# Kernel optimization log

Measured on AMD Instinct MI355X. Metric: run time of the kernel, lower is better.

## Reference

```python
import jax, jax.numpy as jnp
import numpy as np

DIM = 16
HID = 256
BATCH = 8192
N_STEPS = 10      # fixed-step RK4 replaces adaptive dopri5 for a deterministic reference
T0, T1 = 0.0, 1.0
LOG_2PI = float(np.log(2.0 * np.pi))


def setup_inputs() -> dict:
    key = jax.random.key(0)
    ks = jax.random.split(key, 7)

    def lin_w(k, fan_in, fan_out):
        lim = 1.0 / np.sqrt(fan_in)
        return jax.random.uniform(k, (fan_in, fan_out), minval=-lim, maxval=lim, dtype=jnp.float32)

    def lin_b(k, fan_in, fan_out):
        lim = 1.0 / np.sqrt(fan_in)
        return jax.random.uniform(k, (fan_out,), minval=-lim, maxval=lim, dtype=jnp.float32)

    x = jax.random.normal(ks[0], (BATCH, DIM), dtype=jnp.float32)
    return {
        "x": x,
        "W1": lin_w(ks[1], DIM + 1, HID), "b1": lin_b(ks[2], DIM + 1, HID),
        "W2": lin_w(ks[3], HID, HID),     "b2": lin_b(ks[4], HID, HID),
        "W3": lin_w(ks[5], HID, DIM),     "b3": lin_b(ks[6], HID, DIM),
    }


def _mlp(W1, b1, W2, b2, W3, b3, h):
    h = jax.nn.silu(h @ W1 + b1)
    h = jax.nn.silu(h @ W2 + b2)
    return h @ W3 + b3


def reference(x, W1, b1, W2, b2, W3, b3):
    dtype = x.dtype

    def f(t, z):  # time-conditioned vector field f(z, t): [B, d] -> [B, d]
        t_col = jnp.full((z.shape[0], 1), t, dtype=dtype)
        return _mlp(W1, b1, W2, b2, W3, b3, jnp.concatenate([z, t_col], axis=1))

    eye = jnp.eye(DIM, dtype=dtype)

    def f_and_div(t, z):
        fz = f(t, z)
        # exact divergence = trace of Jacobian, via DIM forward-mode JVPs
        def jvp_dir(e):  # e: [d]
            _, jv = jax.jvp(lambda zz: f(t, zz), (z,), (jnp.broadcast_to(e, z.shape),))
            return jv  # [B, d]
        jvs = jax.vmap(jvp_dir)(eye)          # [d, B, d]
        div = jnp.einsum('ibi->b', jvs)       # sum_i dF_i/dz_i
        return fz, div

    dt = jnp.asarray((T1 - T0) / N_STEPS, dtype=dtype)

    def rhs(t, z):
        fz, div = f_and_div(t, z)
        return fz, -div   # dz/dt, dlogp/dt

    def step(state, i):
        z, logp = state
        t = T0 + i * dt
        k1z, k1l = rhs(t, z)
        k2z, k2l = rhs(t + 0.5 * dt, z + 0.5 * dt * k1z)
        k3z, k3l = rhs(t + 0.5 * dt, z + 0.5 * dt * k2z)
        k4z, k4l = rhs(t + dt, z + dt * k3z)
        z = z + (dt / 6.0) * (k1z + 2.0 * k2z + 2.0 * k3z + k4z)
        logp = logp + (dt / 6.0) * (k1l + 2.0 * k2l + 2.0 * k3l + k4l)
        return (z, logp), None

    logp0 = jnp.zeros(x.shape[0], dtype=dtype)
    (z1, logp1), _ = jax.lax.scan(step, (x, logp0), jnp.arange(N_STEPS, dtype=dtype))

    logpz = -0.5 * (jnp.sum(z1 * z1, axis=1) + DIM * LOG_2PI)
    return logpz - logp1
```

## Files before the change

kernel.cpp:

```cpp
#include <hip/hip_runtime.h>

#define DIM 16
#define HID 256
#define NSTEPS 10
#define TILE_B 32
#define NTHR 1024
#define LSH 264

typedef __attribute__((ext_vector_type(8))) short bf16x8;
typedef __attribute__((ext_vector_type(4))) float f32x4;
typedef __attribute__((ext_vector_type(2))) unsigned int u32x2;

__device__ __forceinline__ unsigned short f2bf(float f) {
    unsigned u = __float_as_uint(f);
    u += 0x7fff + ((u >> 16) & 1);
    return (unsigned short)(u >> 16);
}
__device__ __forceinline__ float bfw_lo(unsigned u) { return __uint_as_float(u << 16); }
__device__ __forceinline__ float bfw_hi(unsigned u) { return __uint_as_float(u & 0xffff0000u); }
__device__ __forceinline__ unsigned packtr(float a, float b) {
    return __builtin_amdgcn_perm(__float_as_uint(b), __float_as_uint(a), 0x07060302u);
}
__device__ __forceinline__ void silu_both(float x, float& h, float& d) {
    float s = __builtin_amdgcn_rcpf(1.0f + __expf(-x));
    h = x * s;
    d = fmaf(h, 1.0f - s, s);
}

__global__ void cnf_setup(const float* __restrict__ W1, const float* __restrict__ W2,
                          const float* __restrict__ W3,
                          unsigned short* __restrict__ w2t, unsigned short* __restrict__ mt) {
    const int j = blockIdx.x;
    const int n = threadIdx.x;
    float g = 0.0f;
#pragma unroll
    for (int i = 0; i < DIM; ++i) g = fmaf(W1[i * HID + j], W3[n * DIM + i], g);
    const float w2 = W2[j * HID + n];
    w2t[n * HID + j] = f2bf(w2);
    mt [n * HID + j] = f2bf(w2 * g);
}

__global__ __launch_bounds__(NTHR, 4) void cnf_main(
    const float* __restrict__ x,
    const float* __restrict__ W1, const float* __restrict__ b1,
    const float* __restrict__ b2, const float* __restrict__ b3,
    const unsigned short* __restrict__ w2t, const unsigned short* __restrict__ mt,
    const float* __restrict__ W3, float* __restrict__ out)
{
    __shared__ unsigned short zb[TILE_B][40];
    __shared__ unsigned short w3t[DIM][LSH];
    __shared__ unsigned short h1s[TILE_B][LSH];
    __shared__ unsigned short d1s[TILE_B][LSH];
    __shared__ unsigned short h2s[TILE_B][LSH];
    __shared__ unsigned short d2s[TILE_B][LSH];
    __shared__ float divp[8][TILE_B];
    __shared__ float b2l[HID];
    __shared__ float b3l[DIM];

    const int tid  = (int)threadIdx.x;
    const int lane = tid & 63;
    const int wv   = tid >> 6;
    const int g    = lane >> 4;
    const int r    = lane & 15;
    const int g8   = g * 8;
    const int b0   = (int)blockIdx.x * TILE_B;
    const int swr  = ((r >> 3) & 1) << 4;
    const int zsw  = ((r >> 3) & 1) << 3;
    const int goff = g8 ^ swr;
    const int n0w  = (wv & 7) * 32;

    bf16x8 breg[8][2];
    {
        const unsigned short* Bg = (wv < 8) ? w2t : mt;
#pragma unroll
        for (int k = 0; k < 8; ++k)
#pragma unroll
            for (int nt = 0; nt < 2; ++nt)
                breg[k][nt] = *(const bf16x8*)(Bg + (n0w + nt * 16 + r) * HID + k * 32 + g8);
    }

    bf16x8 w1f;
    {
        const int n = wv * 16 + r;
#pragma unroll
        for (int e = 0; e < 8; ++e) {
            const int k = g8 + e;
            float v = 0.0f;
            if (k < 17)       v = W1[k * HID + n];
            else if (k == 17) v = b1[n];
            w1f[e] = (short)f2bf(v);
        }
    }

    float zb4[4] = {0, 0, 0, 0}, za4[4] = {0, 0, 0, 0};
    if (wv < 2) {
        const f32x4 xv = *(const f32x4*)&x[(b0 + wv * 16 + r) * DIM + 4 * g];
#pragma unroll
        for (int q = 0; q < 4; ++q) zb4[q] = xv[q];
        u32x2 pz = { (unsigned)f2bf(zb4[0]) | ((unsigned)f2bf(zb4[1]) << 16),
                     (unsigned)f2bf(zb4[2]) | ((unsigned)f2bf(zb4[3]) << 16) };
        *(u32x2*)&zb[wv * 16 + r][(4 * g) ^ zsw] = pz;
    }
    if (tid < TILE_B) {
        const int zswi = ((tid >> 3) & 1) << 3;
#pragma unroll
        for (int c = 16; c < 32; ++c)
            zb[tid][c ^ zswi] = (c == 17) ? (unsigned short)0x3F80 : (unsigned short)0;
    }
    if (tid < 512) {
        const int n = tid >> 5, k0 = (tid & 31) * 8;
#pragma unroll
        for (int j = 0; j < 8; ++j) w3t[n][k0 + j] = f2bf(W3[(k0 + j) * DIM + n]);
    }
    if (tid < HID) b2l[tid] = b2[tid];
    if (tid < DIM) b3l[tid] = b3[tid];

    float lacc = 0.0f, logp = 0.0f;
    const float dt = 0.1f, dt6 = dt / 6.0f;

    for (int it = 0; it < NSTEPS * 4; ++it) {
        const int s = it & 3;
        const float wst = (s == 1 || s == 2) ? 2.0f : 1.0f;
        int opq = 0;
        asm volatile("" : "+v"(opq));
        __syncthreads();

        if (wv == 8 && lane < TILE_B && it) {
            const int ps = (it + 3) & 3;
            const float pw = (ps == 1 || ps == 2) ? 2.0f : 1.0f;
            float dv = 0.0f;
#pragma unroll
            for (int w = 0; w < 8; ++w) dv += divp[w][lane];
            lacc = fmaf(-pw, dv, lacc);
            if (ps == 3) { logp = fmaf(dt6, lacc, logp); lacc = 0.0f; }
        }

        {
            const bf16x8 bz0 = *(const bf16x8*)&zb[r][g8 ^ zsw];
            const bf16x8 bz1 = *(const bf16x8*)&zb[16 + r][g8 ^ zsw];
#pragma unroll
            for (int bt = 0; bt < 2; ++bt) {
                f32x4 c = {0.f, 0.f, 0.f, 0.f};
                c = __builtin_amdgcn_mfma_f32_16x16x32_bf16(w1f, bt ? bz1 : bz0, c, 0, 0, 0);
                float h[4], d[4];
#pragma unroll
                for (int q = 0; q < 4; ++q) silu_both(c[q], h[q], d[q]);
                const int row = bt * 16 + r;
                const int col = (wv * 16 + 4 * g) ^ swr;
                u32x2 hv  = { packtr(h[0], h[1]), packtr(h[2], h[3]) };
                u32x2 dv2 = { packtr(d[0], d[1]), packtr(d[2], d[3]) };
                *(u32x2*)&h1s[row][col] = hv;
                *(u32x2*)&d1s[row][col] = dv2;
            }
        }
        __syncthreads();

        f32x4 cc[2][2];
        {
            const unsigned short (*aT)[LSH] = (wv < 8) ? h1s : d1s;
#pragma unroll
            for (int a = 0; a < 2; ++a)
#pragma unroll
                for (int b = 0; b < 2; ++b) cc[a][b] = (f32x4){0.f, 0.f, 0.f, 0.f};
            __builtin_amdgcn_s_setprio(1);
#pragma unroll
            for (int k = 0; k < 8; ++k) {
                bf16x8 af[2];
#pragma unroll
                for (int bt = 0; bt < 2; ++bt)
                    af[bt] = *(const bf16x8*)&aT[bt * 16 + r][k * 32 + goff];
#pragma unroll
                for (int nt = 0; nt < 2; ++nt)
#pragma unroll
                    for (int bt = 0; bt < 2; ++bt)
                        cc[nt][bt] = __builtin_amdgcn_mfma_f32_16x16x32_bf16(breg[k][nt], af[bt], cc[nt][bt], 0, 0, 0);
            }
            __builtin_amdgcn_s_setprio(0);
        }
        if (wv < 8) {
#pragma unroll
            for (int nt = 0; nt < 2; ++nt) {
                const f32x4* bp2 = (const f32x4*)&b2l[n0w + nt * 16 + 4 * g];
                const f32x4 bb = bp2[opq];
#pragma unroll
                for (int bt = 0; bt < 2; ++bt) {
                    float h[4], d[4];
#pragma unroll
                    for (int q = 0; q < 4; ++q) silu_both(cc[nt][bt][q] + bb[q], h[q], d[q]);
                    const int row = bt * 16 + r;
                    const int col = (n0w + nt * 16 + 4 * g) ^ swr;
                    u32x2 hv  = { packtr(h[0], h[1]), packtr(h[2], h[3]) };
                    u32x2 dv2 = { packtr(d[0], d[1]), packtr(d[2], d[3]) };
                    *(u32x2*)&h2s[row][col] = hv;
                    *(u32x2*)&d2s[row][col] = dv2;
                }
            }
        }
        __syncthreads();

        if (wv < 2) {
            __builtin_amdgcn_s_setprio(1);
            const unsigned short* h2row = &h2s[wv * 16 + r][0];
            const unsigned short* w3row = &w3t[r][0];
            f32x4 c3a = {0.f, 0.f, 0.f, 0.f}, c3b = {0.f, 0.f, 0.f, 0.f};
#pragma unroll
            for (int kt = 0; kt < 8; ++kt) {
                const bf16x8 a3  = *(const bf16x8*)(w3row + kt * 32 + g8);
                const bf16x8 bf3 = *(const bf16x8*)(h2row + kt * 32 + goff);
                if (kt & 1) c3b = __builtin_amdgcn_mfma_f32_16x16x32_bf16(a3, bf3, c3b, 0, 0, 0);
                else        c3a = __builtin_amdgcn_mfma_f32_16x16x32_bf16(a3, bf3, c3a, 0, 0, 0);
            }
            const f32x4* bp3 = (const f32x4*)&b3l[4 * g];
            const f32x4 b3v = bp3[opq];
            const float coef = (s == 2) ? dt : 0.5f * dt;
            float zn[4];
#pragma unroll
            for (int q = 0; q < 4; ++q) {
                const float fz = c3a[q] + c3b[q] + b3v[q];
                za4[q] = fmaf(wst, fz, za4[q]);
                if (s < 3) zn[q] = fmaf(coef, fz, zb4[q]);
                else { zb4[q] = fmaf(dt6, za4[q], zb4[q]); zn[q] = zb4[q]; za4[q] = 0.0f; }
            }
            u32x2 pz = { (unsigned)f2bf(zn[0]) | ((unsigned)f2bf(zn[1]) << 16),
                         (unsigned)f2bf(zn[2]) | ((unsigned)f2bf(zn[3]) << 16) };
            *(u32x2*)&zb[wv * 16 + r][(4 * g) ^ zsw] = pz;
            if (wv == 0 && lane < TILE_B) {
                const int it1 = it + 1;
                const int s1 = it1 & 3;
                const float t1 = dt * (float)(it1 >> 2) + ((s1 == 0) ? 0.0f : (s1 == 3) ? dt : 0.5f * dt);
                zb[lane][16 ^ (((lane >> 3) & 1) << 3)] = f2bf(t1);
            }
            __builtin_amdgcn_s_setprio(0);
        } else if (wv >= 8) {
            float p0 = 0.0f, p1 = 0.0f;
#pragma unroll
            for (int nt = 0; nt < 2; ++nt)
#pragma unroll
                for (int bt = 0; bt < 2; ++bt) {
                    const int row = bt * 16 + r;
                    const int col = (n0w + nt * 16 + 4 * g) ^ swr;
                    const u32x2 du = *(const u32x2*)&d2s[row][col];
                    float pp = (bt == 0) ? p0 : p1;
                    pp = fmaf(bfw_lo(du[0]), cc[nt][bt][0], pp);
                    pp = fmaf(bfw_hi(du[0]), cc[nt][bt][1], pp);
                    pp = fmaf(bfw_lo(du[1]), cc[nt][bt][2], pp);
                    pp = fmaf(bfw_hi(du[1]), cc[nt][bt][3], pp);
                    if (bt == 0) p0 = pp; else p1 = pp;
                }
            p0 += __shfl_xor(p0, 16, 64);
            p0 += __shfl_xor(p0, 32, 64);
            p1 += __shfl_xor(p1, 16, 64);
            p1 += __shfl_xor(p1, 32, 64);
            if (g < 2) divp[wv - 8][g * 16 + r] = g ? p1 : p0;
        }
    }

    __syncthreads();
    if (wv == 8 && lane < TILE_B) {
        float dv = 0.0f;
#pragma unroll
        for (int w = 0; w < 8; ++w) dv += divp[w][lane];
        lacc -= dv;
        logp = fmaf(dt6, lacc, logp);
        divp[0][lane] = logp;
    }
    __syncthreads();
    if (wv < 2) {
        float ss = zb4[0] * zb4[0] + zb4[1] * zb4[1] + zb4[2] * zb4[2] + zb4[3] * zb4[3];
        ss += __shfl_xor(ss, 16, 64);
        ss += __shfl_xor(ss, 32, 64);
        if (g == 0) {
            const int row = wv * 16 + r;
            out[b0 + row] = -0.5f * (ss + (float)DIM * 1.8378770664093453f) - divp[0][row];
        }
    }
}

extern "C" void kernel_launch(void* const* d_in, const int* in_sizes, int n_in,
                              void* d_out, int out_size, void* d_ws, size_t ws_size,
                              hipStream_t stream) {
    (void)in_sizes; (void)n_in; (void)out_size; (void)ws_size;
    const float* x  = (const float*)d_in[0];
    const float* W1 = (const float*)d_in[1];
    const float* b1 = (const float*)d_in[2];
    const float* W2 = (const float*)d_in[3];
    const float* b2 = (const float*)d_in[4];
    const float* W3 = (const float*)d_in[5];
    const float* b3 = (const float*)d_in[6];
    unsigned short* w2t = (unsigned short*)d_ws;
    unsigned short* mt  = w2t + HID * HID;

    cnf_setup<<<HID, HID, 0, stream>>>(W1, W2, W3, w2t, mt);
    cnf_main<<<8192 / TILE_B, NTHR, 0, stream>>>(x, W1, b1, b2, b3, w2t, mt, W3, (float*)d_out);
}
```

Before: 194.7 us.

## Fuse third-layer matmul into layer-2 epilogue with per-wave partial sums

```diff
diff --git a/kernel.cpp b/kernel.cpp
--- a/kernel.cpp
+++ b/kernel.cpp
@@ -8,6 +8,7 @@
 #define LSH 264
 
 typedef __attribute__((ext_vector_type(8))) short bf16x8;
+typedef __attribute__((ext_vector_type(4))) short bf16x4;
 typedef __attribute__((ext_vector_type(4))) float f32x4;
 typedef __attribute__((ext_vector_type(2))) unsigned int u32x2;
 
@@ -26,6 +27,21 @@
     h = x * s;
     d = fmaf(h, 1.0f - s, s);
 }
+
+#if defined(__has_builtin) && __has_builtin(__builtin_amdgcn_mfma_f32_16x16x16bf16_1k)
+__device__ __forceinline__ f32x4 mfma16(bf16x4 a, bf16x4 b, f32x4 c) {
+    return __builtin_amdgcn_mfma_f32_16x16x16bf16_1k(a, b, c, 0, 0, 0);
+}
+#else
+__device__ __forceinline__ f32x4 mfma16(bf16x4 a, bf16x4 b, f32x4 c) {
+    asm volatile("s_nop 1\n\t"
+                 "v_mfma_f32_16x16x16_bf16 %0, %1, %2, %0\n\t"
+                 "s_nop 7\n\t"
+                 "s_nop 7"
+                 : "+v"(c) : "v"(a), "v"(b));
+    return c;
+}
+#endif
 
 __global__ void cnf_setup(const float* __restrict__ W1, const float* __restrict__ W2,
                           const float* __restrict__ W3,
@@ -51,11 +67,11 @@
     __shared__ unsigned short w3t[DIM][LSH];
     __shared__ unsigned short h1s[TILE_B][LSH];
     __shared__ unsigned short d1s[TILE_B][LSH];
-    __shared__ unsigned short h2s[TILE_B][LSH];
     __shared__ unsigned short d2s[TILE_B][LSH];
-    __shared__ float divp[8][TILE_B];
-    __shared__ float b2l[HID];
-    __shared__ float b3l[DIM];
+    __shared__ alignas(16) float fzp[8][2][16][20];
+    __shared__ alignas(16) float divp[8][TILE_B];
+    __shared__ alignas(16) float b2l[HID];
+    __shared__ alignas(16) float b3l[DIM];
 
     const int tid  = (int)threadIdx.x;
     const int lane = tid & 63;
@@ -115,6 +131,13 @@
     if (tid < HID) b2l[tid] = b2[tid];
     if (tid < DIM) b3l[tid] = b3[tid];
 
+    __syncthreads();
+    bf16x4 w3f0 = {0, 0, 0, 0}, w3f1 = {0, 0, 0, 0};
+    if (wv < 8) {
+        w3f0 = *(const bf16x4*)&w3t[r][n0w + 4 * g];
+        w3f1 = *(const bf16x4*)&w3t[r][n0w + 16 + 4 * g];
+    }
+
     float lacc = 0.0f, logp = 0.0f;
     const float dt = 0.1f, dt6 = dt / 6.0f;
 
@@ -178,37 +201,38 @@
             __builtin_amdgcn_s_setprio(0);
         }
         if (wv < 8) {
-#pragma unroll
-            for (int nt = 0; nt < 2; ++nt) {
-                const f32x4* bp2 = (const f32x4*)&b2l[n0w + nt * 16 + 4 * g];
-                const f32x4 bb = bp2[opq];
-#pragma unroll
-                for (int bt = 0; bt < 2; ++bt) {
+            const f32x4* bp20 = (const f32x4*)&b2l[n0w + 4 * g];
+            const f32x4* bp21 = (const f32x4*)&b2l[n0w + 16 + 4 * g];
+            const f32x4 bb0 = bp20[opq], bb1 = bp21[opq];
+#pragma unroll
+            for (int bt = 0; bt < 2; ++bt) {
+                f32x4 cp = {0.f, 0.f, 0.f, 0.f};
+#pragma unroll
+                for (int nt = 0; nt < 2; ++nt) {
                     float h[4], d[4];
+                    const f32x4 bb = nt ? bb1 : bb0;
 #pragma unroll
                     for (int q = 0; q < 4; ++q) silu_both(cc[nt][bt][q] + bb[q], h[q], d[q]);
+                    union { unsigned u[2]; bf16x4 v; } hb;
+                    hb.u[0] = packtr(h[0], h[1]);
+                    hb.u[1] = packtr(h[2], h[3]);
                     const int row = bt * 16 + r;
                     const int col = (n0w + nt * 16 + 4 * g) ^ swr;
-                    u32x2 hv  = { packtr(h[0], h[1]), packtr(h[2], h[3]) };
-                    u32x2 dv2 = { packtr(d[0], d[1]), packtr(d[2], d[3]) };
-                    *(u32x2*)&h2s[row][col] = hv;
-                    *(u32x2*)&d2s[row][col] = dv2;
+                    *(u32x2*)&d2s[row][col] = (u32x2){ packtr(d[0], d[1]), packtr(d[2], d[3]) };
+                    cp = mfma16(nt ? w3f1 : w3f0, hb.v, cp);
                 }
+                *(f32x4*)&fzp[wv][bt][r][4 * g] = cp;
             }
         }
         __syncthreads();
 
         if (wv < 2) {
             __builtin_amdgcn_s_setprio(1);
-            const unsigned short* h2row = &h2s[wv * 16 + r][0];
-            const unsigned short* w3row = &w3t[r][0];
-            f32x4 c3a = {0.f, 0.f, 0.f, 0.f}, c3b = {0.f, 0.f, 0.f, 0.f};
-#pragma unroll
-            for (int kt = 0; kt < 8; ++kt) {
-                const bf16x8 a3  = *(const bf16x8*)(w3row + kt * 32 + g8);
-                const bf16x8 bf3 = *(const bf16x8*)(h2row + kt * 32 + goff);
-                if (kt & 1) c3b = __builtin_amdgcn_mfma_f32_16x16x32_bf16(a3, bf3, c3b, 0, 0, 0);
-                else        c3a = __builtin_amdgcn_mfma_f32_16x16x32_bf16(a3, bf3, c3a, 0, 0, 0);
+            f32x4 fa = {0.f, 0.f, 0.f, 0.f}, fb = {0.f, 0.f, 0.f, 0.f};
+#pragma unroll
+            for (int w = 0; w < 8; w += 2) {
+                fa += *(const f32x4*)&fzp[w][wv][r][4 * g];
+                fb += *(const f32x4*)&fzp[w + 1][wv][r][4 * g];
             }
             const f32x4* bp3 = (const f32x4*)&b3l[4 * g];
             const f32x4 b3v = bp3[opq];
@@ -216,7 +240,7 @@
             float zn[4];
 #pragma unroll
             for (int q = 0; q < 4; ++q) {
-                const float fz = c3a[q] + c3b[q] + b3v[q];
+                const float fz = fa[q] + fb[q] + b3v[q];
                 za4[q] = fmaf(wst, fz, za4[q]);
                 if (s < 3) zn[q] = fmaf(coef, fz, zb4[q]);
                 else { zb4[q] = fmaf(dt6, za4[q], zb4[q]); zn[q] = zb4[q]; za4[q] = 0.0f; }
```

New measurement: 195.4 us. Within noise of the previous version (+0.3%).
